# Kernel tuning notes

Hardware: AMD Instinct MI355X
Metric: run time of the kernel (lower is better)

Reference implementation:

```python
import jax, jax.numpy as jnp
import numpy as np

HEADS = 8
DIM_HEAD = 64
EPS = 1e-5  # fp32 eps in ChanLayerNorm


def chan_layer_norm(x, g):
    # x: [b, c, h, w]; normalize over channel dim with biased variance
    mean = jnp.mean(x, axis=1, keepdims=True)
    var = jnp.var(x, axis=1, keepdims=True)
    return (x - mean) * jax.lax.rsqrt(var + EPS) * g[None, :, None, None]


def setup_inputs() -> dict:
    key = jax.random.key(0)
    k1, k2, k3 = jax.random.split(key, 3)
    dim, inner = 512, HEADS * DIM_HEAD
    fmap = jax.random.normal(k1, (16, dim, 64, 64), dtype=jnp.float32)
    # 1x1 conv weights (no bias); scaled like typical init to keep softmax unsaturated
    w_qkv = jax.random.normal(k2, (3 * inner, dim), dtype=jnp.float32) * 0.02
    w_out = jax.random.normal(k3, (dim, inner), dtype=jnp.float32) * 0.02
    g1 = jnp.ones((dim,), dtype=jnp.float32)
    g2 = jnp.ones((dim,), dtype=jnp.float32)
    return {"fmap": fmap, "g1": g1, "w_qkv": w_qkv, "w_out": w_out, "g2": g2}


def reference(fmap, g1, w_qkv, w_out, g2):
    b, c, X, Y = fmap.shape
    h, dh = HEADS, DIM_HEAD
    n = X * Y  # seq_len
    scale = dh ** -0.5

    x = chan_layer_norm(fmap, g1)
    # 1x1 conv == channel matmul: [b, 3*inner, X, Y]
    qkv = jnp.einsum('bcxy,oc->boxy', x, w_qkv)
    q, k, v = jnp.split(qkv, 3, axis=1)

    def to_bhnc(t):
        # b (h c) x y -> b h n c
        return t.reshape(b, h, dh, n).transpose(0, 1, 3, 2)

    q, k, v = map(to_bhnc, (q, k, v))

    q = jax.nn.softmax(q, axis=-1) * scale          # softmax over feature dim
    k = jax.nn.softmax(k, axis=2)                   # softmax over seq dim
    v = v / jnp.linalg.norm(v, axis=-1, keepdims=True)  # l2norm
    inv_sqrt_n = 1.0 / np.sqrt(n)
    k = k * inv_sqrt_n
    v = v * inv_sqrt_n

    context = jnp.einsum('bhnd,bhne->bhde', k, v)   # small d x e context
    out = jnp.einsum('bhnd,bhde->bhne', q, context)  # [b, h, n, dh]

    # b h n d -> b (h d) x y
    out = out.transpose(0, 1, 3, 2).reshape(b, h * dh, X, Y)
    out = jax.nn.gelu(out, approximate=False)
    out = jnp.einsum('bcxy,oc->boxy', out, w_out)
    return chan_layer_norm(out, g2)
```

## Files before the change

kernel.cpp:

```cpp
#include <hip/hip_runtime.h>

typedef unsigned short u16;
typedef __attribute__((ext_vector_type(2))) float f32x2;
typedef __attribute__((ext_vector_type(4))) float f32x4;
typedef __attribute__((ext_vector_type(8))) short s16x8;
typedef __attribute__((ext_vector_type(8))) u16 u16x8;
typedef __attribute__((ext_vector_type(4))) u16 u16x4;

#define NB 16
#define CD 512
#define NS 4096
#define NHD 8

#define SBAR  __builtin_amdgcn_s_barrier()
#define SCHED __builtin_amdgcn_sched_barrier(0)
#define PRIO1 __builtin_amdgcn_s_setprio(1)
#define PRIO0 __builtin_amdgcn_s_setprio(0)

__device__ __forceinline__ float bf2f(u16 u){
  union { unsigned int i; float f; } z; z.i = ((unsigned int)u) << 16; return z.f;
}
__device__ __forceinline__ u16 f2bf(float f){
  union { float f; unsigned int i; } z; z.f = f;
  unsigned int i = z.i;
  return (u16)((i + 0x7fffu + ((i >> 16) & 1u)) >> 16);
}
__device__ __forceinline__ float gelu_f(float x){
  return 0.5f * x * (1.0f + erff(x * 0.70710678118654752440f));
}
__device__ __forceinline__ void gl_lds16(const u16* g, u16* l){
  __builtin_amdgcn_global_load_lds((const __attribute__((address_space(1))) void*)(g),
                                   (__attribute__((address_space(3))) void*)(l), 16, 0, 0);
}

__global__ void prep_w_k(const float* __restrict__ wqkv, const float* __restrict__ g1,
                         const float* __restrict__ wout, u16* __restrict__ w1b,
                         u16* __restrict__ w2b){
  int i = blockIdx.x * 256 + threadIdx.x;
  if (i < 1536*512) {
    w1b[i] = f2bf(wqkv[i] * g1[i & 511]);
  } else {
    int j = i - 1536*512;
    w2b[j] = f2bf(wout[j]);
  }
}

__global__ __launch_bounds__(512) void ln1t_k(const float* __restrict__ fmap,
                                              u16* __restrict__ xlnT){
  int b = blockIdx.y, n0 = blockIdx.x * 32;
  int t = threadIdx.x;
  int lane = t & 63, wv = t >> 6;
  __shared__ u16 Lb[512][40];
  __shared__ u16 Tt[64][36];
  __shared__ float red1[8][8][4], red2[8][8][4];
  __shared__ float mean_s[32], rstd_s[32];

  int ng = t & 7;
  float s1[4] = {0,0,0,0}, s2[4] = {0,0,0,0};
  const float* fb = fmap + ((size_t)b*CD)*NS + n0 + ng*4;
  #pragma unroll
  for (int it = 0; it < 8; ++it){
    int q = it*512 + t;
    int c = q >> 3;
    f32x4 v = *(const f32x4*)&fb[(size_t)c*NS];
    u16x4 pk;
    #pragma unroll
    for (int j = 0; j < 4; ++j){
      pk[j] = f2bf(v[j]);
      s1[j] += v[j]; s2[j] += v[j]*v[j];
    }
    *(u16x4*)&Lb[c][ng*4] = pk;
  }
  #pragma unroll
  for (int off = 8; off < 64; off <<= 1)
    #pragma unroll
    for (int j = 0; j < 4; ++j){
      s1[j] += __shfl_xor(s1[j], off, 64);
      s2[j] += __shfl_xor(s2[j], off, 64);
    }
  if (lane < 8){
    #pragma unroll
    for (int j = 0; j < 4; ++j){ red1[wv][lane][j] = s1[j]; red2[wv][lane][j] = s2[j]; }
  }
  __syncthreads();
  if (t < 32){
    int g = t >> 2, j = t & 3;
    float a = 0.f, bq = 0.f;
    #pragma unroll
    for (int w = 0; w < 8; ++w){ a += red1[w][g][j]; bq += red2[w][g][j]; }
    float mn = a * (1.f/512.f);
    float var = bq * (1.f/512.f) - mn*mn;
    mean_s[t] = mn; rstd_s[t] = rsqrtf(var + 1e-5f);
  }
  __syncthreads();

  for (int ct = 0; ct < 8; ++ct){
    {
      int cl = t >> 3, n4 = (t & 7) * 4;
      u16x4 xv = *(const u16x4*)&Lb[ct*64 + cl][n4];
      u16x4 pk;
      #pragma unroll
      for (int j = 0; j < 4; ++j)
        pk[j] = f2bf((bf2f(xv[j]) - mean_s[n4+j]) * rstd_s[n4+j]);
      *(u16x4*)&Tt[cl][n4] = pk;
    }
    __syncthreads();
    {
      int nr = t >> 4, c4 = t & 15;
      u16x4 w;
      #pragma unroll
      for (int j = 0; j < 4; ++j) w[j] = Tt[c4*4 + j][nr];
      *(u16x4*)&xlnT[((size_t)b*NS + n0 + nr)*CD + ct*64 + c4*4] = w;
    }
    __syncthreads();
  }
}

__global__ __launch_bounds__(512) void gemm1q_k(const u16* __restrict__ A,
                                                const u16* __restrict__ Bm,
                                                u16* __restrict__ Q){
  __shared__ u16 lds[8][8192];
  int bi = blockIdx.x;
  int xcd = bi & 7, r2 = bi >> 3;
  int yy = r2 & 1, gi = r2 >> 1;
  int g  = gi*8 + xcd;
  int x  = g & 15, z = g >> 4;
  int o0 = yy*256, bn0 = x*256;
  int t = threadIdx.x;
  int lane = t & 63, wv = t >> 6;
  int wm = wv >> 2, wn = wv & 3;
  int fr = lane & 15, fg = lane >> 4;
  const u16* Ab = A + (size_t)o0*512;
  const u16* Bb = Bm + ((size_t)z*NS + bn0)*512;
  int li8 = lane >> 3, scn = lane & 7;

  f32x4 acc[8][4];
  #pragma unroll
  for (int i=0;i<8;++i)
    #pragma unroll
    for (int j=0;j<4;++j) acc[i][j] = (f32x4){0.f,0.f,0.f,0.f};
  s16x8 afr[4][2];
  s16x8 bfr[2][2][2];

  auto stH = [&](int slot, int half, int kt){
    #pragma unroll
    for (int it=0; it<2; ++it){
      int li = it*64 + wv*8 + li8;
      int q  = scn ^ (li & 7);
      int row;
      if (half < 2) row = ((li>>6)<<7) + half*64 + (li & 63);
      else          row = ((li>>5)<<6) + (half-2)*32 + (li & 31);
      const u16* G = (half < 2) ? Ab : Bb;
      gl_lds16(G + (size_t)row*512 + kt + q*8, &lds[slot*4+half][it*4096 + wv*512]);
    }
  };
  auto ldA = [&](int slot, int mq){
    #pragma unroll
    for (int mr=0;mr<4;++mr)
      #pragma unroll
      for (int ks=0;ks<2;++ks){
        int li = wm*64 + mr*16 + fr;
        int c8 = (ks*4+fg) ^ (li & 7);
        afr[mr][ks] = *(const s16x8*)&lds[slot*4+mq][li*64 + c8*8];
      }
  };
  auto ldB = [&](int slot, int nq){
    #pragma unroll
    for (int nr=0;nr<2;++nr)
      #pragma unroll
      for (int ks=0;ks<2;++ks){
        int li = wn*32 + nr*16 + fr;
        int c8 = (ks*4+fg) ^ (li & 7);
        bfr[nq][nr][ks] = *(const s16x8*)&lds[slot*4+2+nq][li*64 + c8*8];
      }
  };
  auto mm = [&](int mq, int nq){
    #pragma unroll
    for (int mr=0;mr<4;++mr)
      #pragma unroll
      for (int nr=0;nr<2;++nr)
        #pragma unroll
        for (int ks=0;ks<2;++ks)
          acc[mq*4+mr][nq*2+nr] = __builtin_amdgcn_mfma_f32_16x16x32_bf16(
              afr[mr][ks], bfr[nq][nr][ks], acc[mq*4+mr][nq*2+nr], 0,0,0);
  };

  stH(0,0,0); stH(0,2,0); stH(0,3,0); stH(0,1,0);
  asm volatile("s_waitcnt vmcnt(2)" ::: "memory");
  SBAR; SCHED;

  #pragma unroll
  for (int kt=0; kt<8; ++kt){
    int slot = kt & 1, ns = slot ^ 1, kn = (kt+1)*64;
    bool F = kt < 7;
    ldA(slot,0); ldB(slot,0); ldB(slot,1);
    if (F){ stH(ns,0,kn); stH(ns,2,kn); stH(ns,3,kn); }
    PRIO1; mm(0,0); mm(0,1); PRIO0;
    if (F) asm volatile("s_waitcnt vmcnt(6)" ::: "memory");
    else   asm volatile("s_waitcnt vmcnt(0)" ::: "memory");
    SBAR; SCHED;
    ldA(slot,1);
    if (F) stH(ns,1,kn);
    PRIO1; mm(1,1); mm(1,0); PRIO0;
    if (F) asm volatile("s_waitcnt vmcnt(2)" ::: "memory");
    SBAR; SCHED;
  }

  size_t cb = (size_t)z * 512 * NS;
  #pragma unroll
  for (int mq=0;mq<2;++mq)
    #pragma unroll
    for (int mr=0;mr<4;++mr)
      #pragma unroll
      for (int nq=0;nq<2;++nq)
        #pragma unroll
        for (int nr=0;nr<2;++nr){
          int row = o0 + wm*128 + mq*64 + mr*16 + fg*4;
          int col = bn0 + wn*64 + nq*32 + nr*16 + fr;
          #pragma unroll
          for (int r=0;r<4;++r)
            Q[cb + (size_t)(row+r)*NS + col] = f2bf(acc[mq*4+mr][nq*2+nr][r]);
        }
}

__global__ __launch_bounds__(512) void gemm1kv_k(const u16* __restrict__ A,
                                                 const u16* __restrict__ Bm,
                                                 float* __restrict__ part,
                                                 float* __restrict__ mS){
  __shared__ u16 lds[8][8192];
  int bi = blockIdx.x;
  int xcd = bi & 7, r2 = bi >> 3;
  int hp = r2 & 3, gg = r2 >> 2;
  int g8 = gg*8 + xcd;
  int x  = g8 & 15, z = g8 >> 4;
  int bn0 = x*256;
  int t = threadIdx.x;
  int lane = t & 63, wv = t >> 6;
  int wm = wv >> 2, wn = wv & 3;
  int fr = lane & 15, fg = lane >> 4;
  const u16* Akb = A + (size_t)(512  + hp*128)*512;
  const u16* Avb = A + (size_t)(1024 + hp*128)*512;
  const u16* Bb  = Bm + ((size_t)z*NS + bn0)*512;
  int li8 = lane >> 3, scn = lane & 7;

  f32x4 acc[8][4];
  #pragma unroll
  for (int i=0;i<8;++i)
    #pragma unroll
    for (int j=0;j<4;++j) acc[i][j] = (f32x4){0.f,0.f,0.f,0.f};
  s16x8 afr[4][2];
  s16x8 bfr[2][2][2];

  auto stH = [&](int slot, int half, int kt){
    #pragma unroll
    for (int it=0; it<2; ++it){
      int li = it*64 + wv*8 + li8;
      int q  = scn ^ (li & 7);
      if (half < 2){
        int rr = half*64 + (li & 63);
        const u16* G = it ? Avb : Akb;
        gl_lds16(G + (size_t)rr*512 + kt + q*8, &lds[slot*4+half][it*4096 + wv*512]);
      } else {
        int row = ((li>>5)<<6) + (half-2)*32 + (li & 31);
        gl_lds16(Bb + (size_t)row*512 + kt + q*8, &lds[slot*4+half][it*4096 + wv*512]);
      }
    }
  };
  auto ldA = [&](int slot, int mq){
    #pragma unroll
    for (int mr=0;mr<4;++mr)
      #pragma unroll
      for (int ks=0;ks<2;++ks){
        int li = wm*64 + mr*16 + fr;
        int c8 = (ks*4+fg) ^ (li & 7);
        afr[mr][ks] = *(const s16x8*)&lds[slot*4+mq][li*64 + c8*8];
      }
  };
  auto ldB = [&](int slot, int nq){
    #pragma unroll
    for (int nr=0;nr<2;++nr)
      #pragma unroll
      for (int ks=0;ks<2;++ks){
        int li = wn*32 + nr*16 + fr;
        int c8 = (ks*4+fg) ^ (li & 7);
        bfr[nq][nr][ks] = *(const s16x8*)&lds[slot*4+2+nq][li*64 + c8*8];
      }
  };
  auto mm = [&](int mq, int nq){
    #pragma unroll
    for (int mr=0;mr<4;++mr)
      #pragma unroll
      for (int nr=0;nr<2;++nr)
        #pragma unroll
        for (int ks=0;ks<2;++ks)
          acc[mq*4+mr][nq*2+nr] = __builtin_amdgcn_mfma_f32_16x16x32_bf16(
              afr[mr][ks], bfr[nq][nr][ks], acc[mq*4+mr][nq*2+nr], 0,0,0);
  };

  stH(0,0,0); stH(0,2,0); stH(0,3,0); stH(0,1,0);
  asm volatile("s_waitcnt vmcnt(2)" ::: "memory");
  SBAR; SCHED;

  #pragma unroll
  for (int kt=0; kt<8; ++kt){
    int slot = kt & 1, ns = slot ^ 1, kn = (kt+1)*64;
    bool F = kt < 7;
    ldA(slot,0); ldB(slot,0); ldB(slot,1);
    if (F){ stH(ns,0,kn); stH(ns,2,kn); stH(ns,3,kn); }
    PRIO1; mm(0,0); mm(0,1); PRIO0;
    if (F) asm volatile("s_waitcnt vmcnt(6)" ::: "memory");
    else   asm volatile("s_waitcnt vmcnt(0)" ::: "memory");
    SBAR; SCHED;
    ldA(slot,1);
    if (F) stH(ns,1,kn);
    PRIO1; mm(1,1); mm(1,0); PRIO0;
    if (F) asm volatile("s_waitcnt vmcnt(2)" ::: "memory");
    SBAR; SCHED;
  }

  if (wm == 0){
    #pragma unroll
    for (int mq=0;mq<2;++mq)
      #pragma unroll
      for (int mr=0;mr<4;++mr)
        #pragma unroll
        for (int nj=0;nj<4;++nj){
          int nq = nj>>1, nr = nj&1;
          #pragma unroll
          for (int r=0;r<4;++r){
            int d  = mr*16 + fg*4 + r;
            int nl = wn*64 + nq*32 + nr*16 + fr;
            int hh = nl >> 7, n1 = nl & 127;
            lds[mq*2+hh][d*128 + (n1 ^ ((d&7)<<3))] = f2bf(__expf(acc[mq*4+mr][nj][r]));
          }
        }
  } else {
    float ss[2][4];
    #pragma unroll
    for (int mq=0;mq<2;++mq)
      #pragma unroll
      for (int nj=0;nj<4;++nj){
        float s = 0.f;
        #pragma unroll
        for (int mr=0;mr<4;++mr)
          #pragma unroll
          for (int r=0;r<4;++r){ float v = acc[mq*4+mr][nj][r]; s += v*v; }
        s += __shfl_xor(s, 16, 64);
        s += __shfl_xor(s, 32, 64);
        ss[mq][nj] = rsqrtf(s);
      }
    #pragma unroll
    for (int mq=0;mq<2;++mq)
      #pragma unroll
      for (int mr=0;mr<4;++mr)
        #pragma unroll
        for (int nj=0;nj<4;++nj){
          int nq = nj>>1, nr = nj&1;
          #pragma unroll
          for (int r=0;r<4;++r){
            int e  = mr*16 + fg*4 + r;
            int nl = wn*64 + nq*32 + nr*16 + fr;
            int hh = nl >> 7, n1 = nl & 127;
            lds[4 + mq*2+hh][e*128 + (n1 ^ ((e&7)<<3))] = f2bf(acc[mq*4+mr][nj][r] * ss[mq][nj]);
          }
        }
  }
  __syncthreads();

  int eg = wv >> 2, ej = wv & 3, ksl = ej & 1;
  const u16* KTt = &lds[eg*2 + (ej>>1)][0];
  const u16* VTt = &lds[4 + eg*2 + (ej>>1)][0];
  f32x4 a2[4][4];
  #pragma unroll
  for (int i=0;i<4;++i)
    #pragma unroll
    for (int j=0;j<4;++j) a2[i][j] = (f32x4){0.f,0.f,0.f,0.f};
  #pragma unroll
  for (int ks2=0; ks2<2; ++ks2){
    int kc = ksl*64 + ks2*32 + fg*8;
    s16x8 af[4], bf_[4];
    #pragma unroll
    for (int i=0;i<4;++i){
      int ra = i*16 + fr;
      af[i]  = *(const s16x8*)&KTt[ra*128 + (kc ^ ((ra&7)<<3))];
      bf_[i] = *(const s16x8*)&VTt[ra*128 + (kc ^ ((ra&7)<<3))];
    }
    #pragma unroll
    for (int i=0;i<4;++i)
      #pragma unroll
      for (int j=0;j<4;++j)
        a2[i][j] = __builtin_amdgcn_mfma_f32_16x16x32_bf16(af[i], bf_[j], a2[i][j], 0,0,0);
  }
  float slc = 0.f;
  {
    int d = lane;
    #pragma unroll
    for (int cc=0; cc<8; ++cc){
      int c0 = ksl*64 + cc*8;
      u16x8 vv = *(const u16x8*)&KTt[d*128 + (c0 ^ ((d&7)<<3))];
      #pragma unroll
      for (int jj=0;jj<8;++jj) slc += bf2f(vv[jj]);
    }
  }
  __syncthreads();

  if (ej >= 1){
    float* dbuf = (float*)&lds[eg*3 + (ej-1)][0];
    #pragma unroll
    for (int i=0;i<4;++i)
      #pragma unroll
      for (int j=0;j<4;++j)
        #pragma unroll
        for (int r=0;r<4;++r) dbuf[((i*4+j)*4+r)*64 + lane] = a2[i][j][r];
  }
  ((float*)&lds[6][0])[eg*256 + ej*64 + lane] = slc;
  __syncthreads();

  int bh = z*8 + hp*2 + eg;
  size_t base = (size_t)bh*16 + x;
  if (ej == 0){
    #pragma unroll
    for (int bb=0; bb<3; ++bb){
      float* dbuf = (float*)&lds[eg*3 + bb][0];
      #pragma unroll
      for (int i=0;i<4;++i)
        #pragma unroll
        for (int j=0;j<4;++j)
          #pragma unroll
          for (int r=0;r<4;++r) a2[i][j][r] += dbuf[((i*4+j)*4+r)*64 + lane];
    }
    float* pp = part + base*4096;
    #pragma unroll
    for (int i=0;i<4;++i)
      #pragma unroll
      for (int j=0;j<4;++j)
        #pragma unroll
        for (int r=0;r<4;++r)
          pp[(i*16+fg*4+r)*64 + j*16+fr] = a2[i][j][r];
  } else if (ej == 1){
    float* sB = (float*)&lds[6][0];
    float s = sB[eg*256 + lane] + sB[eg*256 + 64 + lane]
            + sB[eg*256 + 128 + lane] + sB[eg*256 + 192 + lane];
    mS[base*128 + lane]      = 0.0f;
    mS[base*128 + 64 + lane] = s;
  }
}

__global__ void ctxred_k(const float* __restrict__ part, const float* __restrict__ mS,
                         float* __restrict__ ctx){
  int bh = blockIdx.x, t = threadIdx.x;
  __shared__ float fs[16][64];
  if (t < 64){
    int d = t;
    float denom = 0.f;
    #pragma unroll
    for (int c=0;c<16;++c)
      denom += mS[((size_t)bh*16 + c)*128 + 64 + d];
    float inv = 1.0f / (denom * 4096.0f);
    #pragma unroll
    for (int c=0;c<16;++c) fs[c][d] = inv;
  }
  __syncthreads();
  #pragma unroll
  for (int i=0;i<16;++i){
    int idx = t + i*256;
    int d = idx >> 6;
    float s = 0.f;
    #pragma unroll
    for (int ch=0; ch<16; ++ch) s += fs[ch][d] * part[((size_t)bh*16 + ch)*4096 + idx];
    ctx[(size_t)bh*4096 + idx] = s;
  }
}

__global__ __launch_bounds__(512, 2) void gemm2f_k(const u16* __restrict__ A,
                                                   const u16* __restrict__ q,
                                                   const float* __restrict__ ctx,
                                                   const float* __restrict__ g2,
                                                   float* __restrict__ out){
  __shared__ u16 Bh[2][4096];
  __shared__ u16 P[128][72];
  __shared__ u16 cT[64][72];
  __shared__ float invP[128];
  int x = blockIdx.x, z = blockIdx.y;
  int n0 = x*128;
  int t = threadIdx.x;
  int lane = t & 63, wv = t >> 6;
  int wm = wv >> 1, wn = wv & 1;
  int we2 = wv >> 2, nn = wv & 3;
  int fr = lane & 15, fg = lane >> 4;
  const u16* Ab = A;

  f32x4 acc[8][4];
  #pragma unroll
  for (int i=0;i<8;++i)
    #pragma unroll
    for (int j=0;j<4;++j) acc[i][j] = (f32x4){0.f,0.f,0.f,0.f};
  s16x8 afr[4], bfr[4];

  auto ldAg = [&](int h, int kt2, int h2){
    #pragma unroll
    for (int mi=0;mi<4;++mi){
      int R = wm*128 + (h2*4+mi)*16 + fr;
      afr[mi] = *(const s16x8*)&Ab[(size_t)R*512 + h*64 + kt2*32 + fg*8];
    }
  };
  auto ldBh = [&](int kt2){
    #pragma unroll
    for (int nj=0;nj<4;++nj){
      int R = wn*64 + nj*16 + fr;
      int L = R & 63, hh = R >> 6;
      int c8 = (hh*4 + fg) ^ (L & 7);
      bfr[nj] = *(const s16x8*)&Bh[kt2][L*64 + c8*8];
    }
  };
  auto mm16 = [&](int h2){
    #pragma unroll
    for (int mi=0;mi<4;++mi)
      #pragma unroll
      for (int nj=0;nj<4;++nj)
        acc[h2*4+mi][nj] = __builtin_amdgcn_mfma_f32_16x16x32_bf16(
            afr[mi], bfr[nj], acc[h2*4+mi][nj], 0,0,0);
  };

  for (int h = 0; h < 8; ++h){
    const float* cs = ctx + ((size_t)(z*8 + h))*4096;
    #pragma unroll
    for (int i=0;i<8;++i){
      int idx = i*512 + t;
      cT[idx & 63][idx >> 6] = f2bf(cs[idx]);
    }
    {
      int nl = wv*16 + fr;
      const u16* qb = q + ((size_t)(z*512 + h*64 + fg*16))*NS + n0 + nl;
      float p[16];
      float m = -3.0e38f;
      #pragma unroll
      for (int j=0;j<16;++j){ p[j] = bf2f(qb[(size_t)j*NS]); m = fmaxf(m, p[j]); }
      m = fmaxf(m, __shfl_xor(m, 16, 64));
      m = fmaxf(m, __shfl_xor(m, 32, 64));
      float s = 0.f;
      #pragma unroll
      for (int j=0;j<16;++j){ p[j] = __expf(p[j]-m); s += p[j]; }
      s += __shfl_xor(s, 16, 64);
      s += __shfl_xor(s, 32, 64);
      u16x8 pk;
      #pragma unroll
      for (int j=0;j<8;++j) pk[j] = f2bf(p[j]);
      *(u16x8*)&P[nl][fg*16] = pk;
      #pragma unroll
      for (int j=0;j<8;++j) pk[j] = f2bf(p[8+j]);
      *(u16x8*)&P[nl][fg*16+8] = pk;
      if (fg == 0) invP[nl] = 0.125f / s;
    }
    __syncthreads();

    f32x4 a2[2][2];
    #pragma unroll
    for (int i=0;i<2;++i)
      #pragma unroll
      for (int j=0;j<2;++j) a2[i][j] = (f32x4){0.f,0.f,0.f,0.f};
    #pragma unroll
    for (int ks=0; ks<2; ++ks){
      s16x8 afx[2], bfx[2];
      #pragma unroll
      for (int ei=0;ei<2;++ei)
        afx[ei] = *(const s16x8*)&cT[we2*32 + ei*16 + fr][ks*32 + fg*8];
      #pragma unroll
      for (int ni=0;ni<2;++ni)
        bfx[ni] = *(const s16x8*)&P[nn*32 + ni*16 + fr][ks*32 + fg*8];
      #pragma unroll
      for (int ei=0;ei<2;++ei)
        #pragma unroll
        for (int ni=0;ni<2;++ni)
          a2[ei][ni] = __builtin_amdgcn_mfma_f32_16x16x32_bf16(afx[ei], bfx[ni], a2[ei][ni], 0,0,0);
    }
    #pragma unroll
    for (int ei=0;ei<2;++ei)
      #pragma unroll
      for (int ni=0;ni<2;++ni){
        int n = nn*32 + ni*16 + fr;
        float ip = invP[n];
        u16x4 w4;
        #pragma unroll
        for (int r=0;r<4;++r) w4[r] = f2bf(gelu_f(a2[ei][ni][r] * ip));
        int e32 = ei*16 + fg*4;
        int chunk = e32 >> 3, sub = e32 & 7;
        int L = n & 63, hh = n >> 6;
        int c8 = (hh*4 + chunk) ^ (L & 7);
        *(u16x4*)&Bh[we2][L*64 + c8*8 + sub] = w4;
      }
    __syncthreads();

    #pragma unroll
    for (int kt2=0; kt2<2; ++kt2){
      ldBh(kt2);
      ldAg(h,kt2,0); PRIO1; mm16(0); PRIO0;
      ldAg(h,kt2,1); PRIO1; mm16(1); PRIO0;
    }
  }

  __syncthreads();
  float* red1 = (float*)&P[0][0];
  float* red2 = red1 + 512;
  float* ms   = red2 + 512;
  float* rs   = ms + 128;
  float s1[4], s2[4];
  #pragma unroll
  for (int nj=0;nj<4;++nj){
    float a = 0.f, b2 = 0.f;
    #pragma unroll
    for (int mi=0;mi<8;++mi)
      #pragma unroll
      for (int r=0;r<4;++r){ float v = acc[mi][nj][r]; a += v; b2 += v*v; }
    s1[nj] = a; s2[nj] = b2;
  }
  #pragma unroll
  for (int off=16; off<64; off<<=1)
    #pragma unroll
    for (int nj=0;nj<4;++nj){
      s1[nj] += __shfl_xor(s1[nj], off, 64);
      s2[nj] += __shfl_xor(s2[nj], off, 64);
    }
  if (fg == 0){
    #pragma unroll
    for (int nj=0;nj<4;++nj){
      int c = wn*64 + nj*16 + fr;
      red1[wm*128 + c] = s1[nj];
      red2[wm*128 + c] = s2[nj];
    }
  }
  __syncthreads();
  if (t < 128){
    float a  = red1[t] + red1[128+t] + red1[256+t] + red1[384+t];
    float b2 = red2[t] + red2[128+t] + red2[256+t] + red2[384+t];
    float mn = a * (1.f/512.f);
    float var = b2 * (1.f/512.f) - mn*mn;
    ms[t] = mn; rs[t] = rsqrtf(var + 1e-5f);
  }
  __syncthreads();
  float mc[4], rc[4];
  #pragma unroll
  for (int nj=0;nj<4;++nj){
    int c = wn*64 + nj*16 + fr;
    mc[nj] = ms[c]; rc[nj] = rs[c];
  }
  float* ob = out + (size_t)z*CD*NS + n0;
  #pragma unroll
  for (int mi=0;mi<8;++mi)
    #pragma unroll
    for (int r=0;r<4;++r){
      int row = wm*128 + mi*16 + fg*4 + r;
      float gg = g2[row];
      #pragma unroll
      for (int nj=0;nj<4;++nj)
        ob[(size_t)row*NS + wn*64 + nj*16 + fr] = (acc[mi][nj][r] - mc[nj])*rc[nj]*gg;
    }
}

extern "C" void kernel_launch(void* const* d_in, const int* in_sizes, int n_in,
                              void* d_out, int out_size, void* d_ws, size_t ws_size,
                              hipStream_t stream) {
  const float* fmap = (const float*)d_in[0];
  const float* g1   = (const float*)d_in[1];
  const float* wqkv = (const float*)d_in[2];
  const float* wout = (const float*)d_in[3];
  const float* g2   = (const float*)d_in[4];
  float* out = (float*)d_out;

  char* ws = (char*)d_ws;
  size_t off = 0;
  auto alloc = [&](size_t bytes) -> void* {
    void* p = ws + off;
    off += (bytes + 255) & ~(size_t)255;
    return p;
  };
  u16*   q    = (u16*)alloc((size_t)16*512*4096*2);
  u16*   xlnT = (u16*)alloc((size_t)16*4096*512*2);
  float* part = (float*)alloc((size_t)128*16*4096*4);
  float* mS   = (float*)alloc((size_t)128*16*128*4);
  float* ctx  = (float*)alloc((size_t)128*4096*4);
  u16*   w1b  = (u16*)alloc((size_t)1536*512*2);
  u16*   w2b  = (u16*)alloc((size_t)512*512*2);
  if (off > ws_size) return;

  prep_w_k<<<4096, 256, 0, stream>>>(wqkv, g1, wout, w1b, w2b);
  ln1t_k<<<dim3(128,16), 512, 0, stream>>>(fmap, xlnT);
  gemm1q_k<<<512, 512, 0, stream>>>(w1b, xlnT, q);
  gemm1kv_k<<<1024, 512, 0, stream>>>(w1b, xlnT, part, mS);
  ctxred_k<<<128, 256, 0, stream>>>(part, mS, ctx);
  gemm2f_k<<<dim3(32,16), 512, 0, stream>>>(w2b, q, ctx, g2, out);
}
```

Baseline: 311.6 us.

## Stage w_out tiles in LDS via async global-to-LDS double buffering

Instead of each wave loading A (w_out) fragments straight from global memory, the kernel now stages 256x32 bf16 slices into a double-buffered LDS region with direct global-to-LDS loads, issued ahead of the gelu/context phase and waited on with vmcnt. It also changes how the gelu output is split into the two Bh k-halves. The intent is to hide global-load latency behind the preceding compute and to stop the duplicate A fragment reads across waves. In exchange the kernel uses 64KB more LDS and drops the min-2-blocks launch bound, which may reduce occupancy.

```diff
diff --git a/kernel.cpp b/kernel.cpp
--- a/kernel.cpp
+++ b/kernel.cpp
@@ -472,11 +472,12 @@
   }
 }
 
-__global__ __launch_bounds__(512, 2) void gemm2f_k(const u16* __restrict__ A,
-                                                   const u16* __restrict__ q,
-                                                   const float* __restrict__ ctx,
-                                                   const float* __restrict__ g2,
-                                                   float* __restrict__ out){
+__global__ __launch_bounds__(512) void gemm2f_k(const u16* __restrict__ A,
+                                                const u16* __restrict__ q,
+                                                const float* __restrict__ ctx,
+                                                const float* __restrict__ g2,
+                                                float* __restrict__ out){
+  __shared__ u16 Ar[2][16384];
   __shared__ u16 Bh[2][4096];
   __shared__ u16 P[128][72];
   __shared__ u16 cT[64][72];
@@ -488,6 +489,7 @@
   int wm = wv >> 1, wn = wv & 1;
   int we2 = wv >> 2, nn = wv & 3;
   int fr = lane & 15, fg = lane >> 4;
+  int l8 = lane >> 3, c8d = lane & 7;
   const u16* Ab = A;
 
   f32x4 acc[8][4];
@@ -497,11 +499,23 @@
     for (int j=0;j<4;++j) acc[i][j] = (f32x4){0.f,0.f,0.f,0.f};
   s16x8 afr[4], bfr[4];
 
-  auto ldAg = [&](int h, int kt2, int h2){
+  auto stA4 = [&](int slot, int kt){
+    #pragma unroll
+    for (int bt=0; bt<4; ++bt){
+      int L  = bt*64 + wv*8 + l8;
+      int qq = c8d ^ (l8 & 7);
+      int r  = (qq >> 2)*256 + L;
+      int col = kt + (qq & 3)*8;
+      gl_lds16(Ab + (size_t)r*512 + col, &Ar[slot][(bt*64 + wv*8)*64]);
+    }
+  };
+  auto ldA = [&](int slot, int h2){
     #pragma unroll
     for (int mi=0;mi<4;++mi){
       int R = wm*128 + (h2*4+mi)*16 + fr;
-      afr[mi] = *(const s16x8*)&Ab[(size_t)R*512 + h*64 + kt2*32 + fg*8];
+      int L = R & 255, half = R >> 8;
+      int c8 = (half*4 + fg) ^ (L & 7);
+      afr[mi] = *(const s16x8*)&Ar[slot][L*64 + c8*8];
     }
   };
   auto ldBh = [&](int kt2){
@@ -522,6 +536,8 @@
             afr[mi], bfr[nj], acc[h2*4+mi][nj], 0,0,0);
   };
 
+  stA4(0, 0);
+
   for (int h = 0; h < 8; ++h){
     const float* cs = ctx + ((size_t)(z*8 + h))*4096;
     #pragma unroll
@@ -553,6 +569,7 @@
       if (fg == 0) invP[nl] = 0.125f / s;
     }
     __syncthreads();
+    stA4(1, (2*h+1)*32);
 
     f32x4 a2[2][2];
     #pragma unroll
@@ -583,24 +600,31 @@
         u16x4 w4;
         #pragma unroll
         for (int r=0;r<4;++r) w4[r] = f2bf(gelu_f(a2[ei][ni][r] * ip));
-        int e32 = ei*16 + fg*4;
-        int chunk = e32 >> 3, sub = e32 & 7;
+        int e32 = we2*32 + ei*16 + fg*4;
+        int kt2w = e32 >> 5;
+        int ec = e32 & 31;
+        int chunk = ec >> 3, sub = ec & 7;
         int L = n & 63, hh = n >> 6;
         int c8 = (hh*4 + chunk) ^ (L & 7);
-        *(u16x4*)&Bh[we2][L*64 + c8*8 + sub] = w4;
+        *(u16x4*)&Bh[kt2w][L*64 + c8*8 + sub] = w4;
       }
+    asm volatile("s_waitcnt vmcnt(4)" ::: "memory");
     __syncthreads();
-
-    #pragma unroll
-    for (int kt2=0; kt2<2; ++kt2){
-      ldBh(kt2);
-      ldAg(h,kt2,0); PRIO1; mm16(0); PRIO0;
-      ldAg(h,kt2,1); PRIO1; mm16(1); PRIO0;
-    }
-  }
-
-  __syncthreads();
-  float* red1 = (float*)&P[0][0];
+    ldA(0,0); ldBh(0);
+    PRIO1; mm16(0); PRIO0;
+    ldA(0,1);
+    PRIO1; mm16(1); PRIO0;
+    asm volatile("s_waitcnt vmcnt(0)" ::: "memory");
+    __syncthreads();
+    if (h < 7) stA4(0, (2*h+2)*32);
+    ldA(1,0); ldBh(1);
+    PRIO1; mm16(0); PRIO0;
+    ldA(1,1);
+    PRIO1; mm16(1); PRIO0;
+  }
+
+  __syncthreads();
+  float* red1 = (float*)&Ar[0][0];
   float* red2 = red1 + 512;
   float* ms   = red2 + 512;
   float* rs   = ms + 128;
```

Result: faster. 280.1 us (-10.1%).
